# Optimization experiments

Measured on AMD Instinct MI355X. Metric: run time of the kernel, lower is better.

The kernel has to match this reference:

```python
import jax, jax.numpy as jnp
import numpy as np

B, ROI, T, H, F, DH = 8, 90, 200, 3, 64, 64
BN_EPS = 1e-5
R = ROI * H


def setup_inputs() -> dict:
    key = jax.random.key(0)
    ks = jax.random.split(key, 8)
    x = jax.random.normal(ks[0], (B, ROI, T, H, F), jnp.float32)
    a_vals = jax.random.normal(ks[1], (B, ROI, T, H, ROI), jnp.float32)
    keep = (jax.random.uniform(ks[2], (B, ROI, T, H, ROI)) < 0.2).astype(jnp.float32)
    a = a_vals * keep
    s = 0.05
    gnn_W1 = jax.random.normal(ks[3], (H, F, F), jnp.float32) * s
    gnn_b1 = jnp.zeros((H, F), jnp.float32)
    gnn_g1 = jnp.ones((H, F), jnp.float32)
    gnn_be1 = jnp.zeros((H, F), jnp.float32)
    gnn_W2 = jax.random.normal(ks[4], (H, F, F), jnp.float32) * s
    gnn_b2 = jnp.zeros((H, F), jnp.float32)
    gnn_g2 = jnp.ones((H, F), jnp.float32)
    gnn_be2 = jnp.zeros((H, F), jnp.float32)
    eps_param = jnp.zeros((H,), jnp.float32)  # spGNN epsilon, init 0
    Wih = jax.random.normal(ks[5], (R, 3 * DH, F), jnp.float32) * s
    Whh = jax.random.normal(ks[6], (R, 3 * DH, DH), jnp.float32) * s
    bih = jnp.zeros((R, 3 * DH), jnp.float32)
    bhh = jnp.zeros((R, 3 * DH), jnp.float32)
    return dict(x=x, a=a, eps_param=eps_param,
                gnn_W1=gnn_W1, gnn_b1=gnn_b1, gnn_g1=gnn_g1, gnn_be1=gnn_be1,
                gnn_W2=gnn_W2, gnn_b2=gnn_b2, gnn_g2=gnn_g2, gnn_be2=gnn_be2,
                Wih=Wih, Whh=Whh, bih=bih, bhh=bhh)


def _bn(z, g, be):
    # BatchNorm1d in training mode: stats over the (b*T*roi) flattened batch dim,
    # i.e. axes (0,1,2) of (b, roi, T, H, F); biased variance, eps=1e-5.
    m = z.mean(axis=(0, 1, 2), keepdims=True)
    v = z.var(axis=(0, 1, 2), keepdims=True)
    return g * (z - m) * jax.lax.rsqrt(v + BN_EPS) + be


def reference(x, a, eps_param, gnn_W1, gnn_b1, gnn_g1, gnn_be1,
              gnn_W2, gnn_b2, gnn_g2, gnn_be2, Wih, Whh, bih, bhh):
    # --- spGNN per hop h (block-diagonal sparse mm == per-(b,t) masked matmul) ---
    mask = (a != 0).astype(x.dtype)                      # binary adjacency (b,roi,T,H,roi)
    agg = jnp.einsum('bithj,bjthf->bithf', mask, x)      # sparse.mm aggregation
    v = agg + eps_param[None, None, None, :, None] * x   # + epsilon * x
    z = jnp.einsum('bithf,hfg->bithg', v, gnn_W1) + gnn_b1
    z = jax.nn.elu(_bn(z, gnn_g1, gnn_be1))
    z = jnp.einsum('bithf,hfg->bithg', z, gnn_W2) + gnn_b2
    z = jax.nn.elu(_bn(z, gnn_g2, gnn_be2))
    z = jax.nn.relu(z)
    # --- 270 independent GRUs, batched via grouped weights + scan over time ---
    # rearrange 'b roi T H F -> b (roi H) T F'
    xr = jnp.transpose(z, (0, 1, 3, 2, 4)).reshape(B, R, T, F)
    xs = jnp.moveaxis(xr, 2, 0)                          # (T, b, R, F)
    h0 = jnp.zeros((B, R, DH), x.dtype)

    def step(h, xt):
        gi = jnp.einsum('brf,rgf->brg', xt, Wih) + bih   # (b, R, 3*DH)
        gh = jnp.einsum('brd,rgd->brg', h, Whh) + bhh
        ir, iz, inn = jnp.split(gi, 3, axis=-1)          # torch gate order: r, z, n
        hr, hz, hn = jnp.split(gh, 3, axis=-1)
        r = jax.nn.sigmoid(ir + hr)
        u = jax.nn.sigmoid(iz + hz)
        n = jnp.tanh(inn + r * hn)
        hn_ = (1.0 - u) * n + u * h
        return hn_, hn_

    _, ys = jax.lax.scan(step, h0, xs)                   # (T, b, R, DH)
    out = jnp.moveaxis(ys, 0, 2)                         # (b, R, T, DH)
    # rearrange 'b (roi H) T F -> b roi T H F'
    out = out.reshape(B, ROI, H, T, DH)
    out = jnp.transpose(out, (0, 1, 3, 2, 4))            # (b, roi, T, H, DH)
    return out
```

## Files before the change

kernel.cpp:

```cpp
#include <hip/hip_runtime.h>
#include <cstdint>

#define B_   8
#define ROI_ 90
#define T_   200
#define H_   3
#define F_   64
#define DH_  64
#define R_   270
#define NBN  144000.0f

__device__ __forceinline__ float elu_f(float x) { return x > 0.f ? x : expm1f(x); }
__device__ __forceinline__ float sigm_f(float x) { return 1.f / (1.f + __expf(-x)); }
__device__ __forceinline__ float tanh_f(float x) {
    float xc = fminf(fmaxf(x, -30.f), 30.f);
    float e = __expf(-2.f * xc);
    return (1.f - e) / (1.f + e);
}
__device__ __forceinline__ void fma4(float4& acc, float s, const float4 v) {
    acc.x = fmaf(s, v.x, acc.x); acc.y = fmaf(s, v.y, acc.y);
    acc.z = fmaf(s, v.z, acc.z); acc.w = fmaf(s, v.w, acc.w);
}
__device__ __forceinline__ float dot4(const float4 a, const float4 b) {
    return fmaf(a.x, b.x, fmaf(a.y, b.y, fmaf(a.z, b.z, a.w * b.w)));
}

__global__ __launch_bounds__(256) void k_layer1(
    const float* __restrict__ x, const float* __restrict__ a,
    const float* __restrict__ eps_param, const float* __restrict__ W1,
    const float* __restrict__ b1, float* __restrict__ zbuf,
    float* __restrict__ sum1, float* __restrict__ sq1)
{
    __shared__ __align__(16) char smem[16384 + 26112 + 17280];
    float* wlds = (float*)smem;
    float* xsv  = (float*)(smem + 16384);
    unsigned short* msk = (unsigned short*)(smem + 16384 + 26112);
    float* red = (float*)msk;

    int bid = blockIdx.x;
    int h = bid % 3;
    int t = (bid / 3) % 200;
    int b = bid / 600;
    int tid = threadIdx.x;

    {
        const float4* wsrc = (const float4*)(W1 + h * 4096);
        for (int idx = tid; idx < 1024; idx += 256)
            *(float4*)&wlds[idx * 4] = wsrc[idx];
    }
    {
        size_t xb = ((((size_t)b * 90) * 200 + t) * 3 + h) * 64;
        for (int idx = tid; idx < 1440; idx += 256) {
            int j = idx >> 4, fq = idx & 15;
            float4 v = *(const float4*)(x + xb + (size_t)j * 38400 + fq * 4);
            *(float4*)&xsv[j * 68 + fq * 4] = v;
        }
    }
    {
        size_t ab = ((((size_t)b * 90) * 200 + t) * 3 + h) * 90;
        for (int idx = tid; idx < 8640; idx += 256) {
            int i = idx / 90, j = idx - i * 90;
            unsigned short mv = 0;
            if (i < 90) {
                float av = a[ab + (size_t)i * 54000 + j];
                mv = (av != 0.f) ? (unsigned short)0x3F80 : (unsigned short)0;
            }
            msk[idx] = mv;
        }
    }
    __syncthreads();

    int fg = tid & 15, ig = tid >> 4;
    int f0 = fg * 4;
    float4 acc[6];
#pragma unroll
    for (int k = 0; k < 6; k++) acc[k] = make_float4(0.f, 0.f, 0.f, 0.f);
    for (int j = 0; j < 90; j++) {
        float4 xv = *(float4*)&xsv[j * 68 + f0];
#pragma unroll
        for (int k = 0; k < 6; k++) {
            unsigned int mb = msk[(ig + 16 * k) * 90 + j];
            float m = __uint_as_float(mb << 16);
            fma4(acc[k], m, xv);
        }
    }
    float ep = eps_param[h];
#pragma unroll
    for (int k = 0; k < 6; k++) {
        int i = ig + 16 * k;
        if (i < 90) {
            float4 xv = *(float4*)&xsv[i * 68 + f0];
            fma4(acc[k], ep, xv);
        }
    }
    __syncthreads();
#pragma unroll
    for (int k = 0; k < 6; k++) {
        int i = ig + 16 * k;
        if (i < 90) *(float4*)&xsv[i * 68 + f0] = acc[k];
    }
    __syncthreads();

    int gg = tid & 15, im = tid >> 4;
    int g0 = gg * 4;
    float4 bv = *(const float4*)(b1 + h * 64 + g0);
    float4 z[6];
#pragma unroll
    for (int k = 0; k < 6; k++) z[k] = bv;
    for (int fq = 0; fq < 16; fq++) {
        float4 wv0 = *(float4*)&wlds[(fq * 4 + 0) * 64 + g0];
        float4 wv1 = *(float4*)&wlds[(fq * 4 + 1) * 64 + g0];
        float4 wv2 = *(float4*)&wlds[(fq * 4 + 2) * 64 + g0];
        float4 wv3 = *(float4*)&wlds[(fq * 4 + 3) * 64 + g0];
#pragma unroll
        for (int k = 0; k < 6; k++) {
            float4 vv = *(float4*)&xsv[(im + 16 * k) * 68 + fq * 4];
            fma4(z[k], vv.x, wv0); fma4(z[k], vv.y, wv1);
            fma4(z[k], vv.z, wv2); fma4(z[k], vv.w, wv3);
        }
    }
    float4 s = make_float4(0, 0, 0, 0), s2 = make_float4(0, 0, 0, 0);
    size_t zb = ((((size_t)b * 90) * 200 + t) * 3 + h) * 64;
#pragma unroll
    for (int k = 0; k < 6; k++) {
        int i = im + 16 * k;
        if (i < 90) {
            *(float4*)(zbuf + zb + (size_t)i * 38400 + g0) = z[k];
            s.x += z[k].x; s.y += z[k].y; s.z += z[k].z; s.w += z[k].w;
            s2.x += z[k].x * z[k].x; s2.y += z[k].y * z[k].y;
            s2.z += z[k].z * z[k].z; s2.w += z[k].w * z[k].w;
        }
    }
    *(float4*)&red[im * 64 + g0] = s;
    *(float4*)&red[1024 + im * 64 + g0] = s2;
    __syncthreads();
    if (tid < 64) {
        float S = 0.f, S2 = 0.f;
        for (int q = 0; q < 16; q++) { S += red[q * 64 + tid]; S2 += red[1024 + q * 64 + tid]; }
        atomicAdd(&sum1[h * 64 + tid], S);
        atomicAdd(&sq1[h * 64 + tid], S2);
    }
}

__global__ void k_bnfin(const float* __restrict__ sum, const float* __restrict__ sq,
                        const float* __restrict__ g, const float* __restrict__ be,
                        float* __restrict__ scale, float* __restrict__ shift)
{
    int c = threadIdx.x;
    if (c < 192) {
        float mean = sum[c] / NBN;
        float var = fmaxf(sq[c] / NBN - mean * mean, 0.f);
        float inv = rsqrtf(var + 1e-5f);
        float sc = g[c] * inv;
        scale[c] = sc;
        shift[c] = fmaf(-mean, sc, be[c]);
    }
}

__global__ __launch_bounds__(256) void k_layer2(
    float* zbuf, const float* __restrict__ W2, const float* __restrict__ b2,
    const float* __restrict__ scale1, const float* __restrict__ shift1,
    float* __restrict__ sum2, float* __restrict__ sq2)
{
    __shared__ __align__(16) float wlds[4096];
    __shared__ __align__(16) float zt[96 * 68];
    __shared__ float red[2048];

    int bid = blockIdx.x;
    int h = bid % 3;
    int t = (bid / 3) % 200;
    int b = bid / 600;
    int tid = threadIdx.x;

    {
        const float4* wsrc = (const float4*)(W2 + h * 4096);
        for (int idx = tid; idx < 1024; idx += 256)
            *(float4*)&wlds[idx * 4] = wsrc[idx];
    }
    size_t zb = ((((size_t)b * 90) * 200 + t) * 3 + h) * 64;
    for (int idx = tid; idx < 1440; idx += 256) {
        int j = idx >> 4, fq = idx & 15;
        float4 v = *(const float4*)(zbuf + zb + (size_t)j * 38400 + fq * 4);
        float4 sc = *(const float4*)(scale1 + h * 64 + fq * 4);
        float4 sh = *(const float4*)(shift1 + h * 64 + fq * 4);
        v.x = elu_f(fmaf(v.x, sc.x, sh.x));
        v.y = elu_f(fmaf(v.y, sc.y, sh.y));
        v.z = elu_f(fmaf(v.z, sc.z, sh.z));
        v.w = elu_f(fmaf(v.w, sc.w, sh.w));
        *(float4*)&zt[j * 68 + fq * 4] = v;
    }
    __syncthreads();

    int gg = tid & 15, im = tid >> 4;
    int g0 = gg * 4;
    float4 bv = *(const float4*)(b2 + h * 64 + g0);
    float4 z[6];
#pragma unroll
    for (int k = 0; k < 6; k++) z[k] = bv;
    for (int fq = 0; fq < 16; fq++) {
        float4 wv0 = *(float4*)&wlds[(fq * 4 + 0) * 64 + g0];
        float4 wv1 = *(float4*)&wlds[(fq * 4 + 1) * 64 + g0];
        float4 wv2 = *(float4*)&wlds[(fq * 4 + 2) * 64 + g0];
        float4 wv3 = *(float4*)&wlds[(fq * 4 + 3) * 64 + g0];
#pragma unroll
        for (int k = 0; k < 6; k++) {
            float4 vv = *(float4*)&zt[(im + 16 * k) * 68 + fq * 4];
            fma4(z[k], vv.x, wv0); fma4(z[k], vv.y, wv1);
            fma4(z[k], vv.z, wv2); fma4(z[k], vv.w, wv3);
        }
    }
    float4 s = make_float4(0, 0, 0, 0), s2 = make_float4(0, 0, 0, 0);
#pragma unroll
    for (int k = 0; k < 6; k++) {
        int i = im + 16 * k;
        if (i < 90) {
            *(float4*)(zbuf + zb + (size_t)i * 38400 + g0) = z[k];
            s.x += z[k].x; s.y += z[k].y; s.z += z[k].z; s.w += z[k].w;
            s2.x += z[k].x * z[k].x; s2.y += z[k].y * z[k].y;
            s2.z += z[k].z * z[k].z; s2.w += z[k].w * z[k].w;
        }
    }
    *(float4*)&red[im * 64 + g0] = s;
    *(float4*)&red[1024 + im * 64 + g0] = s2;
    __syncthreads();
    if (tid < 64) {
        float S = 0.f, S2 = 0.f;
        for (int q = 0; q < 16; q++) { S += red[q * 64 + tid]; S2 += red[1024 + q * 64 + tid]; }
        atomicAdd(&sum2[h * 64 + tid], S);
        atomicAdd(&sq2[h * 64 + tid], S2);
    }
}

__global__ __launch_bounds__(256) void k_giproj(
    const float* __restrict__ zin, const float* __restrict__ Wih,
    const float* __restrict__ bih, const float* __restrict__ scale2,
    const float* __restrict__ shift2, float* __restrict__ gi)
{
    __shared__ __align__(16) float wl[192 * 68];
    __shared__ __align__(16) float zl[40 * 68];
    __shared__ float bsc[64], bsh[64];

    int bid = blockIdx.x;
    int r = bid >> 2, tq = bid & 3;
    int roi = r / 3, h = r - roi * 3;
    int tid = threadIdx.x;

    if (tid < 64) { bsc[tid] = scale2[h * 64 + tid]; bsh[tid] = shift2[h * 64 + tid]; }
    {
        const float4* wsrc = (const float4*)(Wih + (size_t)r * 12288);
        for (int idx = tid; idx < 3072; idx += 256) {
            int g = idx >> 4, fq = idx & 15;
            *(float4*)&wl[g * 68 + fq * 4] = wsrc[idx];
        }
    }
    int gg = tid & 31, rg = tid >> 5;
    float bihv[6];
#pragma unroll
    for (int k = 0; k < 6; k++) bihv[k] = bih[r * 192 + gg + 32 * k];

    for (int ci = 0; ci < 10; ci++) {
        int t0 = tq * 50 + ci * 5;
        __syncthreads();
        for (int idx = tid; idx < 640; idx += 256) {
            int row = idx >> 4, fq = idx & 15;
            int dt = row >> 3, bb = row & 7;
            size_t addr = ((((size_t)bb * 90 + roi) * 200 + (t0 + dt)) * 3 + h) * 64 + fq * 4;
            float4 v = *(const float4*)(zin + addr);
            float4 sc = *(const float4*)&bsc[fq * 4];
            float4 sh = *(const float4*)&bsh[fq * 4];
            v.x = fmaxf(fmaf(v.x, sc.x, sh.x), 0.f);
            v.y = fmaxf(fmaf(v.y, sc.y, sh.y), 0.f);
            v.z = fmaxf(fmaf(v.z, sc.z, sh.z), 0.f);
            v.w = fmaxf(fmaf(v.w, sc.w, sh.w), 0.f);
            *(float4*)&zl[row * 68 + fq * 4] = v;
        }
        __syncthreads();
        float acc[6][5];
#pragma unroll
        for (int k = 0; k < 6; k++)
#pragma unroll
            for (int rr = 0; rr < 5; rr++) acc[k][rr] = 0.f;
        for (int fq = 0; fq < 16; fq++) {
            float4 wv[6];
#pragma unroll
            for (int k = 0; k < 6; k++) wv[k] = *(float4*)&wl[(gg + 32 * k) * 68 + fq * 4];
#pragma unroll
            for (int rr = 0; rr < 5; rr++) {
                float4 zv = *(float4*)&zl[(rg * 5 + rr) * 68 + fq * 4];
#pragma unroll
                for (int k = 0; k < 6; k++) {
                    acc[k][rr] = fmaf(zv.x, wv[k].x, acc[k][rr]);
                    acc[k][rr] = fmaf(zv.y, wv[k].y, acc[k][rr]);
                    acc[k][rr] = fmaf(zv.z, wv[k].z, acc[k][rr]);
                    acc[k][rr] = fmaf(zv.w, wv[k].w, acc[k][rr]);
                }
            }
        }
#pragma unroll
        for (int rr = 0; rr < 5; rr++) {
            int row = rg * 5 + rr; int dt = row >> 3, bb = row & 7;
            size_t gb = (((size_t)(t0 + dt) * 270 + r) * 8 + bb) * 192 + gg;
#pragma unroll
            for (int k = 0; k < 6; k++) gi[gb + 32 * k] = acc[k][rr] + bihv[k];
        }
    }
}

__global__ __launch_bounds__(256) void k_gru(
    const float* __restrict__ gi, const float* __restrict__ Whh,
    const float* __restrict__ bhh, float* __restrict__ out)
{
    __shared__ __align__(16) float staged[64 * 68];
    __shared__ __align__(16) float red[1536];
    __shared__ float hl[2 * 68];

    int bid = blockIdx.x;
    int r = bid >> 2, bq = bid & 3;
    int roi = r / 3, h = r - roi * 3;
    int b0 = bq * 2;
    int tid = threadIdx.x;
    int gt = tid & 63, dg = tid >> 6;

    float4 wreg[3][4];
    const float4* wsrc = (const float4*)(Whh + (size_t)r * 12288);
    for (int c = 0; c < 3; c++) {
        __syncthreads();
        for (int idx = tid; idx < 1024; idx += 256) {
            int gl = idx >> 4, fq = idx & 15;
            *(float4*)&staged[gl * 68 + fq * 4] = wsrc[c * 1024 + idx];
        }
        __syncthreads();
#pragma unroll
        for (int dq = 0; dq < 4; dq++)
            wreg[c][dq] = *(float4*)&staged[gt * 68 + dg * 16 + dq * 4];
    }

    int lb = tid & 1, d = tid >> 1;
    float bh0 = 0.f, bh1 = 0.f, bh2 = 0.f;
    const float* gib = gi + ((size_t)r * 8 + b0 + lb) * 192;
    size_t ob = 0;
    if (tid < 128) {
        bh0 = bhh[r * 192 + d];
        bh1 = bhh[r * 192 + 64 + d];
        bh2 = bhh[r * 192 + 128 + d];
        ob = ((((size_t)(b0 + lb) * 90 + roi) * 200) * 3 + h) * 64 + d;
    }
    if (tid < 136) hl[tid] = 0.f;
    __syncthreads();

    const size_t gstep = 270ull * 8 * 192;
    for (int t = 0; t < 200; t++) {
        float a00 = 0.f, a01 = 0.f, a02 = 0.f, a10 = 0.f, a11 = 0.f, a12 = 0.f;
#pragma unroll
        for (int dq = 0; dq < 4; dq++) {
            float4 h0 = *(float4*)&hl[dg * 16 + dq * 4];
            float4 h1 = *(float4*)&hl[68 + dg * 16 + dq * 4];
            float4 w0 = wreg[0][dq], w1 = wreg[1][dq], w2 = wreg[2][dq];
            a00 += dot4(w0, h0); a01 += dot4(w1, h0); a02 += dot4(w2, h0);
            a10 += dot4(w0, h1); a11 += dot4(w1, h1); a12 += dot4(w2, h1);
        }
        int rb = (dg * 64 + gt) * 6;
        *(float2*)&red[rb + 0] = make_float2(a00, a10);
        *(float2*)&red[rb + 2] = make_float2(a01, a11);
        *(float2*)&red[rb + 4] = make_float2(a02, a12);
        __syncthreads();
        if (tid < 128) {
            int base = d * 6 + lb;
            float ghr = red[base]     + red[384 + base]     + red[768 + base]     + red[1152 + base]     + bh0;
            float ghz = red[base + 2] + red[384 + base + 2] + red[768 + base + 2] + red[1152 + base + 2] + bh1;
            float ghn = red[base + 4] + red[384 + base + 4] + red[768 + base + 4] + red[1152 + base + 4] + bh2;
            const float* gp = gib + (size_t)t * gstep;
            float rr_ = sigm_f(gp[d] + ghr);
            float uu  = sigm_f(gp[64 + d] + ghz);
            float nn  = tanh_f(fmaf(rr_, ghn, gp[128 + d]));
            float hold = hl[lb * 68 + d];
            float hnew = fmaf(uu, hold - nn, nn);
            hl[lb * 68 + d] = hnew;
            out[ob + (size_t)t * 192] = hnew;
        }
        __syncthreads();
    }
}

extern "C" void kernel_launch(void* const* d_in, const int* in_sizes, int n_in,
                              void* d_out, int out_size, void* d_ws, size_t ws_size,
                              hipStream_t stream)
{
    const float* x   = (const float*)d_in[0];
    const float* a   = (const float*)d_in[1];
    const float* eps = (const float*)d_in[2];
    const float* W1  = (const float*)d_in[3];
    const float* b1  = (const float*)d_in[4];
    const float* g1  = (const float*)d_in[5];
    const float* be1 = (const float*)d_in[6];
    const float* W2  = (const float*)d_in[7];
    const float* b2  = (const float*)d_in[8];
    const float* g2  = (const float*)d_in[9];
    const float* be2 = (const float*)d_in[10];
    const float* Wih = (const float*)d_in[11];
    const float* Whh = (const float*)d_in[12];
    const float* bih = (const float*)d_in[13];
    const float* bhh = (const float*)d_in[14];
    float* out = (float*)d_out;

    float* wsf = (float*)d_ws;
    float* sum1 = wsf,        *sq1 = wsf + 192;
    float* sum2 = wsf + 384,  *sq2 = wsf + 576;
    float* scale1 = wsf + 768,  *shift1 = wsf + 960;
    float* scale2 = wsf + 1152, *shift2 = wsf + 1344;
    float* zbuf = wsf + 2048;
    float* gi   = zbuf + 27648000ull;

    hipMemsetAsync(wsf, 0, 768 * sizeof(float), stream);
    hipLaunchKernelGGL(k_layer1, dim3(4800), dim3(256), 0, stream,
                       x, a, eps, W1, b1, zbuf, sum1, sq1);
    hipLaunchKernelGGL(k_bnfin, dim3(1), dim3(256), 0, stream,
                       sum1, sq1, g1, be1, scale1, shift1);
    hipLaunchKernelGGL(k_layer2, dim3(4800), dim3(256), 0, stream,
                       zbuf, W2, b2, scale1, shift1, sum2, sq2);
    hipLaunchKernelGGL(k_bnfin, dim3(1), dim3(256), 0, stream,
                       sum2, sq2, g2, be2, scale2, shift2);
    hipLaunchKernelGGL(k_giproj, dim3(1080), dim3(256), 0, stream,
                       zbuf, Wih, bih, scale2, shift2, gi);
    hipLaunchKernelGGL(k_gru, dim3(1080), dim3(256), 0, stream,
                       gi, Whh, bhh, out);
}
```

Measured before the change: 1.379 ms.

## Restructure GRU recurrence to one wavefront per batch with register-resident weights

The GRU kernel now assigns one wavefront per batch element and one lane per hidden unit. Each lane keeps its full 192-weight slice of Whh in registers and does the whole dot product itself, so the shared-memory cross-thread reduction and both per-step block barriers go away; the hidden state is exchanged through a per-wave LDS buffer. It also prefetches the next step's input-gate values and halves the grid. The cost is very high register pressure (about 192 VGPRs just for weights) and reliance on ordered LDS access within a wavefront instead of explicit barriers.

Result: slower. 3.723 ms (+170.0%).

```diff
diff --git a/kernel.cpp b/kernel.cpp
--- a/kernel.cpp
+++ b/kernel.cpp
@@ -9,6 +9,7 @@
 #define DH_  64
 #define R_   270
 #define NBN  144000.0f
+#define GSTEP (270ull * 8 * 192)
 
 __device__ __forceinline__ float elu_f(float x) { return x > 0.f ? x : expm1f(x); }
 __device__ __forceinline__ float sigm_f(float x) { return 1.f / (1.f + __expf(-x)); }
@@ -306,79 +307,72 @@
     }
 }
 
-__global__ __launch_bounds__(256) void k_gru(
+__global__ __launch_bounds__(256, 2) void k_gru(
     const float* __restrict__ gi, const float* __restrict__ Whh,
     const float* __restrict__ bhh, float* __restrict__ out)
 {
-    __shared__ __align__(16) float staged[64 * 68];
-    __shared__ __align__(16) float red[1536];
-    __shared__ float hl[2 * 68];
+    __shared__ __align__(16) float stg[64 * 68];
+    __shared__ __align__(16) float hbuf[4][64];
 
     int bid = blockIdx.x;
-    int r = bid >> 2, bq = bid & 3;
+    int r = bid >> 1, bq = bid & 1;
     int roi = r / 3, h = r - roi * 3;
-    int b0 = bq * 2;
     int tid = threadIdx.x;
-    int gt = tid & 63, dg = tid >> 6;
-
-    float4 wreg[3][4];
+    int w = tid >> 6, l = tid & 63;
+    int b = bq * 4 + w;
+
+    float4 wreg[3][16];
     const float4* wsrc = (const float4*)(Whh + (size_t)r * 12288);
+#pragma unroll
     for (int c = 0; c < 3; c++) {
         __syncthreads();
         for (int idx = tid; idx < 1024; idx += 256) {
             int gl = idx >> 4, fq = idx & 15;
-            *(float4*)&staged[gl * 68 + fq * 4] = wsrc[c * 1024 + idx];
+            *(float4*)&stg[gl * 68 + fq * 4] = wsrc[c * 1024 + idx];
         }
         __syncthreads();
 #pragma unroll
-        for (int dq = 0; dq < 4; dq++)
-            wreg[c][dq] = *(float4*)&staged[gt * 68 + dg * 16 + dq * 4];
-    }
-
-    int lb = tid & 1, d = tid >> 1;
-    float bh0 = 0.f, bh1 = 0.f, bh2 = 0.f;
-    const float* gib = gi + ((size_t)r * 8 + b0 + lb) * 192;
-    size_t ob = 0;
-    if (tid < 128) {
-        bh0 = bhh[r * 192 + d];
-        bh1 = bhh[r * 192 + 64 + d];
-        bh2 = bhh[r * 192 + 128 + d];
-        ob = ((((size_t)(b0 + lb) * 90 + roi) * 200) * 3 + h) * 64 + d;
-    }
-    if (tid < 136) hl[tid] = 0.f;
-    __syncthreads();
-
-    const size_t gstep = 270ull * 8 * 192;
+        for (int q = 0; q < 16; q++)
+            wreg[c][q] = *(float4*)&stg[l * 68 + q * 4];
+    }
+
+    float bh0 = bhh[r * 192 + l];
+    float bh1 = bhh[r * 192 + 64 + l];
+    float bh2 = bhh[r * 192 + 128 + l];
+
+    const float* gp0 = gi + ((size_t)r * 8 + b) * 192 + l;
+    float* op = out + ((((size_t)b * 90 + roi) * 200) * 3 + h) * 64 + l;
+
+    hbuf[w][l] = 0.f;
+    float hreg = 0.f;
+
+    float gr = gp0[0], gz = gp0[64], gn = gp0[128];
+
     for (int t = 0; t < 200; t++) {
-        float a00 = 0.f, a01 = 0.f, a02 = 0.f, a10 = 0.f, a11 = 0.f, a12 = 0.f;
-#pragma unroll
-        for (int dq = 0; dq < 4; dq++) {
-            float4 h0 = *(float4*)&hl[dg * 16 + dq * 4];
-            float4 h1 = *(float4*)&hl[68 + dg * 16 + dq * 4];
-            float4 w0 = wreg[0][dq], w1 = wreg[1][dq], w2 = wreg[2][dq];
-            a00 += dot4(w0, h0); a01 += dot4(w1, h0); a02 += dot4(w2, h0);
-            a10 += dot4(w0, h1); a11 += dot4(w1, h1); a12 += dot4(w2, h1);
-        }
-        int rb = (dg * 64 + gt) * 6;
-        *(float2*)&red[rb + 0] = make_float2(a00, a10);
-        *(float2*)&red[rb + 2] = make_float2(a01, a11);
-        *(float2*)&red[rb + 4] = make_float2(a02, a12);
-        __syncthreads();
-        if (tid < 128) {
-            int base = d * 6 + lb;
-            float ghr = red[base]     + red[384 + base]     + red[768 + base]     + red[1152 + base]     + bh0;
-            float ghz = red[base + 2] + red[384 + base + 2] + red[768 + base + 2] + red[1152 + base + 2] + bh1;
-            float ghn = red[base + 4] + red[384 + base + 4] + red[768 + base + 4] + red[1152 + base + 4] + bh2;
-            const float* gp = gib + (size_t)t * gstep;
-            float rr_ = sigm_f(gp[d] + ghr);
-            float uu  = sigm_f(gp[64 + d] + ghz);
-            float nn  = tanh_f(fmaf(rr_, ghn, gp[128 + d]));
-            float hold = hl[lb * 68 + d];
-            float hnew = fmaf(uu, hold - nn, nn);
-            hl[lb * 68 + d] = hnew;
-            out[ob + (size_t)t * 192] = hnew;
-        }
-        __syncthreads();
+        float s0 = 0.f, s1 = 0.f, s2 = 0.f, s3 = 0.f, s4 = 0.f, s5 = 0.f;
+#pragma unroll
+        for (int q = 0; q < 16; q += 2) {
+            float4 h0 = *(float4*)&hbuf[w][q * 4];
+            float4 h1 = *(float4*)&hbuf[w][q * 4 + 4];
+            s0 += dot4(wreg[0][q], h0); s1 += dot4(wreg[0][q + 1], h1);
+            s2 += dot4(wreg[1][q], h0); s3 += dot4(wreg[1][q + 1], h1);
+            s4 += dot4(wreg[2][q], h0); s5 += dot4(wreg[2][q + 1], h1);
+        }
+        float grn = 0.f, gzn = 0.f, gnn = 0.f;
+        if (t < 199) {
+            const float* gq = gp0 + (size_t)(t + 1) * GSTEP;
+            grn = gq[0]; gzn = gq[64]; gnn = gq[128];
+        }
+        float ghr = s0 + s1 + bh0;
+        float ghz = s2 + s3 + bh1;
+        float ghn = s4 + s5 + bh2;
+        float rr = sigm_f(gr + ghr);
+        float uu = sigm_f(gz + ghz);
+        float nn = tanh_f(fmaf(rr, ghn, gn));
+        hreg = fmaf(uu, hreg - nn, nn);
+        hbuf[w][l] = hreg;
+        op[(size_t)t * 192] = hreg;
+        gr = grn; gz = gzn; gn = gnn;
     }
 }
 
@@ -422,6 +416,6 @@
                        sum2, sq2, g2, be2, scale2, shift2);
     hipLaunchKernelGGL(k_giproj, dim3(1080), dim3(256), 0, stream,
                        zbuf, Wih, bih, scale2, shift2, gi);
-    hipLaunchKernelGGL(k_gru, dim3(1080), dim3(256), 0, stream,
+    hipLaunchKernelGGL(k_gru, dim3(540), dim3(256), 0, stream,
                        gi, Whh, bhh, out);
 }
```
